# Kernel tuning notes

Measured on AMD Instinct MI355X. Metric: run time of the kernel, lower is better.

Reference implementation:

```python
import jax, jax.numpy as jnp
import numpy as np

EPS = 1e-5
NUM_HEADS = 8


def setup_inputs() -> dict:
    key = jax.random.key(0)
    ks = jax.random.split(key, 4)
    B, C, H, W = 16, 512, 32, 32
    x = jax.random.normal(ks[0], (B, C, H, W), dtype=jnp.float32)
    gn_w = jnp.ones((C,), dtype=jnp.float32)
    gn_b = jnp.zeros((C,), dtype=jnp.float32)
    # 1x1 conv weights stored as [out_ch, in_ch] (kernel dims squeezed)
    qkv_w = jax.random.normal(ks[1], (3 * C, C), dtype=jnp.float32) * (1.0 / np.sqrt(C))
    qkv_b = jnp.zeros((3 * C,), dtype=jnp.float32)
    proj_w = jax.random.normal(ks[2], (C, C), dtype=jnp.float32) * (1.0 / np.sqrt(C))
    proj_b = jnp.zeros((C,), dtype=jnp.float32)
    return {"x": x, "gn_w": gn_w, "gn_b": gn_b, "qkv_w": qkv_w,
            "qkv_b": qkv_b, "proj_w": proj_w, "proj_b": proj_b}


def _group_norm(x, w, b, groups):
    B, C, H, W = x.shape
    xg = x.reshape(B, groups, C // groups, H, W)
    mu = jnp.mean(xg, axis=(2, 3, 4), keepdims=True)
    var = jnp.var(xg, axis=(2, 3, 4), keepdims=True)
    xn = ((xg - mu) * jax.lax.rsqrt(var + EPS)).reshape(B, C, H, W)
    return xn * w[None, :, None, None] + b[None, :, None, None]


def reference(x, gn_w, gn_b, qkv_w, qkv_b, proj_w, proj_b):
    B, C, H, W = x.shape
    heads = NUM_HEADS
    d = C // heads
    residual = x
    xn = _group_norm(x, gn_w, gn_b, heads)
    # 1x1 conv == channel matmul
    qkv = jnp.einsum('oc,bchw->bohw', qkv_w, xn) + qkv_b[None, :, None, None]
    q, k, v = jnp.split(qkv, 3, axis=1)  # each [B, C, H, W]
    q = q.reshape(B, heads, d, H * W)
    k = k.reshape(B, heads, d, H * W)
    v = v.reshape(B, heads, d, H * W)
    scale = 1.0 / np.sqrt(d).astype(np.float32)
    attn = jnp.einsum('bhcn,bhcm->bhnm', q, k) * scale  # [B,h,N,N]
    attn = jax.nn.softmax(attn, axis=-1)
    out = jnp.einsum('bhnm,bhcm->bhcn', attn, v).reshape(B, C, H, W)
    out = jnp.einsum('oc,bchw->bohw', proj_w, out) + proj_b[None, :, None, None]
    return residual + out
```

## Files before the change

kernel.cpp:

```cpp
#include <hip/hip_runtime.h>
#include <hip/hip_bf16.h>
#include <math.h>

typedef short bf16x8 __attribute__((ext_vector_type(8)));
typedef short bf16x4 __attribute__((ext_vector_type(4)));
typedef float f32x4  __attribute__((ext_vector_type(4)));
#define MFMA16(a,b,c) __builtin_amdgcn_mfma_f32_16x16x32_bf16(a,b,c,0,0,0)

#if __has_builtin(__builtin_amdgcn_mfma_f32_16x16x16bf16_1k)
#define HAVE_MFMA16X16 1
#define MFMAK16(a,b,c) __builtin_amdgcn_mfma_f32_16x16x16bf16_1k(a,b,c,0,0,0)
#else
#define HAVE_MFMA16X16 0
#endif

#define EPSF 1e-5f
#define QSC 0.18033688f

#if __has_builtin(__builtin_amdgcn_exp2f)
#define EXP2(x) __builtin_amdgcn_exp2f(x)
#else
#define EXP2(x) exp2f(x)
#endif

__device__ __forceinline__ unsigned int pk2n(float a, float b){
  __hip_bfloat162 h = __float22bfloat162_rn(make_float2(a, b));
  return *reinterpret_cast<unsigned int*>(&h);
}
__device__ __forceinline__ unsigned short bfn(float f){
  __hip_bfloat16 h = __float2bfloat16(f);
  return *reinterpret_cast<unsigned short*>(&h);
}
__device__ __forceinline__ float4 ld4(const float* p){ return *reinterpret_cast<const float4*>(p); }
__device__ __forceinline__ void st4(float* p, float4 v){ *reinterpret_cast<float4*>(p) = v; }

__device__ __forceinline__ void gl_lds16(const unsigned short* g, unsigned short* l){
  __builtin_amdgcn_global_load_lds(
      (const __attribute__((address_space(1))) unsigned int*)g,
      (__attribute__((address_space(3))) unsigned int*)l, 16, 0, 0);
}

__global__ __launch_bounds__(256) void wcvt_k(const float* __restrict__ src,
                                              unsigned int* __restrict__ dst){
  int i = blockIdx.x * 256 + threadIdx.x;
  float4 v = reinterpret_cast<const float4*>(src)[i];
  uint2 r; r.x = pk2n(v.x, v.y); r.y = pk2n(v.z, v.w);
  reinterpret_cast<uint2*>(dst)[i] = r;
}

__global__ __launch_bounds__(512) void gn_fused_k(const float* __restrict__ x,
                                                  const float* __restrict__ gnw,
                                                  const float* __restrict__ gnb,
                                                  unsigned short* __restrict__ xnT){
  __shared__ float Xl[2][64*65];
  __shared__ float red[16];
  int blk = blockIdx.x;
  int b = blk >> 3, g = blk & 7;
  int tid = threadIdx.x;
  const float4* p4 = reinterpret_cast<const float4*>(x + (size_t)blk * 65536);
  float s1 = 0.f, s2 = 0.f;
  for(int i = tid; i < 16384; i += 512){
    float4 v = p4[i];
    s1 += (v.x + v.y) + (v.z + v.w);
    s2 += v.x*v.x + v.y*v.y + v.z*v.z + v.w*v.w;
  }
  #pragma unroll
  for(int off = 32; off; off >>= 1){ s1 += __shfl_xor(s1, off); s2 += __shfl_xor(s2, off); }
  if((tid & 63) == 0){ red[tid >> 6] = s1; red[8 + (tid >> 6)] = s2; }
  __syncthreads();
  float a = 0.f, b2 = 0.f;
  #pragma unroll
  for(int w = 0; w < 8; w++){ a += red[w]; b2 += red[8 + w]; }
  float mean = a * (1.f / 65536.f);
  float rstd = rsqrtf(b2 * (1.f / 65536.f) - mean * mean + EPSF);
  int half = tid >> 8, t256 = tid & 255;
  int nq = t256 & 15, rr = t256 >> 4;
  int c0 = g * 64;
  for(int it = 0; it < 8; it++){
    int n0 = (it*2 + half) * 64;
    __syncthreads();
    #pragma unroll
    for(int p = 0; p < 4; p++){
      int cl = p * 16 + rr, c = c0 + cl;
      float s = rstd * gnw[c], t = gnb[c] - mean * s;
      float4 v = ld4(x + ((size_t)(b*512 + c))*1024 + n0 + 4*nq);
      Xl[half][(4*nq+0)*65 + cl] = v.x*s + t;
      Xl[half][(4*nq+1)*65 + cl] = v.y*s + t;
      Xl[half][(4*nq+2)*65 + cl] = v.z*s + t;
      Xl[half][(4*nq+3)*65 + cl] = v.w*s + t;
    }
    __syncthreads();
    int n = t256 >> 2, cq = t256 & 3;
    float f[16];
    #pragma unroll
    for(int k = 0; k < 16; k++) f[k] = Xl[half][n*65 + 16*cq + k];
    uint4 w0, w1;
    w0.x = pk2n(f[0],f[1]);  w0.y = pk2n(f[2],f[3]);  w0.z = pk2n(f[4],f[5]);  w0.w = pk2n(f[6],f[7]);
    w1.x = pk2n(f[8],f[9]);  w1.y = pk2n(f[10],f[11]);w1.z = pk2n(f[12],f[13]);w1.w = pk2n(f[14],f[15]);
    unsigned short* dp = xnT + ((size_t)(b*1024 + n0 + n))*512 + c0 + 16*cq;
    *reinterpret_cast<uint4*>(dp)     = w0;
    *reinterpret_cast<uint4*>(dp + 8) = w1;
  }
}


__global__ __launch_bounds__(256) void qkv_mm(const unsigned short* __restrict__ A,
                                              const unsigned short* __restrict__ Bx,
                                              const float* __restrict__ bias,
                                              unsigned short* __restrict__ T,
                                              unsigned short* __restrict__ V){
  __shared__ __align__(16) unsigned short As[128*64], Bs[128*64];
  int tid = threadIdx.x;
  int n0 = blockIdx.x*128, o0 = blockIdx.y*128, b = blockIdx.z;
  int wid = tid >> 6, wr = wid >> 1, wc = wid & 1, ln = tid & 15, g = (tid >> 4) & 3;
  int l = tid & 63;
  int rsw = (ln & 7) << 3;
  int srow = 32*wid + (l >> 3);
  int scol = (((l & 7) ^ (l >> 3)) << 3);
  const unsigned short* Ag = A  + (size_t)(o0 + srow)*512 + scol;
  const unsigned short* Bg = Bx + ((size_t)(b*1024 + n0 + srow))*512 + scol;
  unsigned short* Asw = As + (32*wid)*64;
  unsigned short* Bsw = Bs + (32*wid)*64;
  f32x4 acc[4][4] = {};
  for(int k0 = 0; k0 < 512; k0 += 64){
    __syncthreads();
    #pragma unroll
    for(int c = 0; c < 4; c++){
      gl_lds16(Ag + (size_t)(8*c)*512 + k0, Asw + (8*c)*64);
      gl_lds16(Bg + (size_t)(8*c)*512 + k0, Bsw + (8*c)*64);
    }
    __syncthreads();
    #pragma unroll
    for(int kh = 0; kh < 2; kh++){
      int ro = (kh*32 + 8*g) ^ rsw;
      bf16x8 af[4], bfv[4];
      #pragma unroll
      for(int mf = 0; mf < 4; mf++)
        af[mf] = *reinterpret_cast<const bf16x8*>(&As[(wr*64 + 16*mf + ln)*64 + ro]);
      #pragma unroll
      for(int nf = 0; nf < 4; nf++)
        bfv[nf] = *reinterpret_cast<const bf16x8*>(&Bs[(wc*64 + 16*nf + ln)*64 + ro]);
      #pragma unroll
      for(int mf = 0; mf < 4; mf++)
        #pragma unroll
        for(int nf = 0; nf < 4; nf++)
          acc[mf][nf] = MFMA16(af[mf], bfv[nf], acc[mf][nf]);
    }
  }
  int obase = o0 + wr*64, nbase = n0 + wc*64;
  __syncthreads();
  unsigned short* scr = (wid < 2 ? As : Bs) + (wid & 1) * 2560;
  float sc = (obase < 512) ? QSC : 1.0f;
  if(obase < 1024){
    #pragma unroll
    for(int h2 = 0; h2 < 2; h2++){
      asm volatile("s_waitcnt lgkmcnt(0)" ::: "memory");
      __builtin_amdgcn_sched_barrier(0);
      #pragma unroll
      for(int mf2 = 0; mf2 < 2; mf2++){
        int mf = 2*h2 + mf2;
        int og = obase + 16*mf + 4*g;
        float b0 = bias[og], b1 = bias[og+1], b2 = bias[og+2], b3 = bias[og+3];
        #pragma unroll
        for(int nf = 0; nf < 4; nf++){
          uint2 pr;
          pr.x = pk2n((acc[mf][nf][0]+b0)*sc, (acc[mf][nf][1]+b1)*sc);
          pr.y = pk2n((acc[mf][nf][2]+b2)*sc, (acc[mf][nf][3]+b3)*sc);
          *reinterpret_cast<uint2*>(&scr[(16*nf + ln)*40 + 16*mf2 + 4*g]) = pr;
        }
      }
      asm volatile("s_waitcnt lgkmcnt(0)" ::: "memory");
      __builtin_amdgcn_sched_barrier(0);
      const unsigned short* rp = &scr[l*40];
      uint4 r0 = *reinterpret_cast<const uint4*>(rp);
      uint4 r1 = *reinterpret_cast<const uint4*>(rp+8);
      uint4 r2 = *reinterpret_cast<const uint4*>(rp+16);
      uint4 r3 = *reinterpret_cast<const uint4*>(rp+24);
      unsigned short* dp = T + ((size_t)(b*1024 + nbase + l))*1024 + obase + 32*h2;
      *reinterpret_cast<uint4*>(dp)    = r0;
      *reinterpret_cast<uint4*>(dp+8)  = r1;
      *reinterpret_cast<uint4*>(dp+16) = r2;
      *reinterpret_cast<uint4*>(dp+24) = r3;
    }
  } else {
    #pragma unroll
    for(int h2 = 0; h2 < 2; h2++){
      asm volatile("s_waitcnt lgkmcnt(0)" ::: "memory");
      __builtin_amdgcn_sched_barrier(0);
      #pragma unroll
      for(int nf2 = 0; nf2 < 2; nf2++){
        int nf = 2*h2 + nf2;
        #pragma unroll
        for(int mf = 0; mf < 4; mf++){
          int og = obase + 16*mf + 4*g;
          #pragma unroll
          for(int r = 0; r < 4; r++)
            scr[(16*mf + 4*g + r)*40 + 16*nf2 + ln] = bfn(acc[mf][nf][r] + bias[og+r]);
        }
      }
      asm volatile("s_waitcnt lgkmcnt(0)" ::: "memory");
      __builtin_amdgcn_sched_barrier(0);
      const unsigned short* rp = &scr[l*40];
      uint4 r0 = *reinterpret_cast<const uint4*>(rp);
      uint4 r1 = *reinterpret_cast<const uint4*>(rp+8);
      uint4 r2 = *reinterpret_cast<const uint4*>(rp+16);
      uint4 r3 = *reinterpret_cast<const uint4*>(rp+24);
      unsigned short* dp = V + ((size_t)(b*512 + obase - 1024 + l))*1024 + nbase + 32*h2;
      *reinterpret_cast<uint4*>(dp)    = r0;
      *reinterpret_cast<uint4*>(dp+8)  = r1;
      *reinterpret_cast<uint4*>(dp+16) = r2;
      *reinterpret_cast<uint4*>(dp+24) = r3;
    }
  }
}

__global__ __launch_bounds__(256) void attn_bf_k(const unsigned short* __restrict__ T,
                                                 const unsigned short* __restrict__ V,
                                                 unsigned short* __restrict__ attT){
  __shared__ __align__(16) unsigned short KT[2][64*64];
  __shared__ __align__(16) unsigned short Vt[2][64*64];
#if !HAVE_MFMA16X16
  __shared__ __align__(16) unsigned int   Pl[4*16*32];
#endif
  int tid = threadIdx.x;
  int id = blockIdx.x;
  int bh = (id >> 7) * 8 + (id & 7);
  int n0 = ((id >> 3) & 15) * 64;
  int b = bh >> 3, h = bh & 7;
  int wq = tid >> 6, ln = tid & 15, g = (tid >> 4) & 3;
  int l = tid & 63;
  int nl = n0 + wq*16 + ln;
  const unsigned short* Tb = T + ((size_t)b << 20);
  bf16x8 qf0 = *reinterpret_cast<const bf16x8*>(Tb + (size_t)nl*1024 + h*64 + 8*g);
  bf16x8 qf1 = *reinterpret_cast<const bf16x8*>(Tb + (size_t)nl*1024 + h*64 + 32 + 8*g);
  f32x4 acc[4] = {};
  float l_part = 0.f;
  const unsigned short* kg = Tb + 512 + h*64;
  const unsigned short* vg = V + ((size_t)(b*512 + h*64))*1024;
  int swz  = (((l & 7) << 3) ^ ((l >> 3) << 3));
  const unsigned short* ksrc = kg + (size_t)(wq*16 + (l>>3))*1024 + swz;
  const unsigned short* vsrc = vg + (size_t)(wq*16 + (l>>3))*1024 + swz;
  int rsw = (ln & 7) << 3;
  int ro0 = (8*g) ^ rsw, ro1 = (32 + 8*g) ^ rsw;
#if HAVE_MFMA16X16
  int vcol[4];
  #pragma unroll
  for(int mf = 0; mf < 4; mf++)
    vcol[mf] = (((2*mf + (g>>1)) ^ (ln & 7)) << 3) + 4*(g & 1);
#else
  int pbase = wq*512 + ln*32;
  int psw = (ln & 7) << 2;
#endif
  {
    unsigned short* kb = &KT[0][wq*16*64];
    unsigned short* vb = &Vt[0][wq*16*64];
    gl_lds16(ksrc,            kb);
    gl_lds16(ksrc + 8*1024,   kb + 8*64);
    gl_lds16(vsrc,            vb);
    gl_lds16(vsrc + 8*1024,   vb + 8*64);
  }
  __syncthreads();
  for(int t = 0; t < 16; t++){
    int buf = t & 1;
    if(t < 15){
      int m1 = (t + 1) * 64;
      unsigned short* kb = &KT[buf^1][wq*16*64];
      unsigned short* vb = &Vt[buf^1][wq*16*64];
      gl_lds16(ksrc + (size_t)m1*1024,          kb);
      gl_lds16(ksrc + (size_t)(m1+8)*1024,      kb + 8*64);
      gl_lds16(vsrc + m1,                       vb);
      gl_lds16(vsrc + 8*1024 + m1,              vb + 8*64);
    }
    f32x4 sf[4];
    #pragma unroll
    for(int mf = 0; mf < 4; mf++){
      bf16x8 a0 = *reinterpret_cast<const bf16x8*>(&KT[buf][(16*mf + ln)*64 + ro0]);
      bf16x8 a1 = *reinterpret_cast<const bf16x8*>(&KT[buf][(16*mf + ln)*64 + ro1]);
      f32x4 z = {0.f, 0.f, 0.f, 0.f};
      z = MFMA16(a0, qf0, z);
      sf[mf] = MFMA16(a1, qf1, z);
    }
    float p[16];
    #pragma unroll
    for(int mf = 0; mf < 4; mf++)
      #pragma unroll
      for(int r = 0; r < 4; r++){
        float v = EXP2(sf[mf][r]);
        p[mf*4 + r] = v;
        l_part += v;
      }
#if HAVE_MFMA16X16
    bf16x4 pb[4];
    #pragma unroll
    for(int mf = 0; mf < 4; mf++){
      union { uint2 u; bf16x4 h; } cv;
      cv.u.x = pk2n(p[4*mf + 0], p[4*mf + 1]);
      cv.u.y = pk2n(p[4*mf + 2], p[4*mf + 3]);
      pb[mf] = cv.h;
    }
    #pragma unroll
    for(int cf = 0; cf < 4; cf++){
      #pragma unroll
      for(int mf = 0; mf < 4; mf++){
        bf16x4 va = *reinterpret_cast<const bf16x4*>(&Vt[buf][(16*cf + ln)*64 + vcol[mf]]);
        acc[cf] = MFMAK16(va, pb[mf], acc[cf]);
      }
    }
#else
    #pragma unroll
    for(int mt = 0; mt < 4; mt++){
      Pl[pbase + ((8*mt + 2*g + 0) ^ psw)] = pk2n(p[4*mt + 0], p[4*mt + 1]);
      Pl[pbase + ((8*mt + 2*g + 1) ^ psw)] = pk2n(p[4*mt + 2], p[4*mt + 3]);
    }
    asm volatile("s_waitcnt lgkmcnt(0)" ::: "memory");
    __builtin_amdgcn_sched_barrier(0);
    union { uint4 u; bf16x8 hv; } pb0, pb1;
    pb0.u = *reinterpret_cast<const uint4*>(&Pl[pbase + ((4*g) ^ psw)]);
    pb1.u = *reinterpret_cast<const uint4*>(&Pl[pbase + ((16 + 4*g) ^ psw)]);
    #pragma unroll
    for(int cf = 0; cf < 4; cf++){
      bf16x8 v0 = *reinterpret_cast<const bf16x8*>(&Vt[buf][(16*cf + ln)*64 + ro0]);
      bf16x8 v1 = *reinterpret_cast<const bf16x8*>(&Vt[buf][(16*cf + ln)*64 + ro1]);
      acc[cf] = MFMA16(v0, pb0.hv, acc[cf]);
      acc[cf] = MFMA16(v1, pb1.hv, acc[cf]);
    }
#endif
    __syncthreads();
  }
  float lsum = l_part;
  lsum += __shfl_xor(lsum, 16);
  lsum += __shfl_xor(lsum, 32);
  float inv = 1.f / lsum;
  unsigned short* op = attT + ((size_t)(b*1024 + nl))*512 + h*64;
  #pragma unroll
  for(int cf = 0; cf < 4; cf++){
    uint2 pr;
    pr.x = pk2n(acc[cf][0]*inv, acc[cf][1]*inv);
    pr.y = pk2n(acc[cf][2]*inv, acc[cf][3]*inv);
    *reinterpret_cast<uint2*>(op + 16*cf + 4*g) = pr;
  }
}

__global__ __launch_bounds__(256) void proj_mm(const unsigned short* __restrict__ A,
                                               const unsigned short* __restrict__ Bx,
                                               const float* __restrict__ bias,
                                               const float* __restrict__ resid,
                                               float* __restrict__ out){
  __shared__ __align__(16) unsigned short As[128*64], Bs[128*64];
  int tid = threadIdx.x;
  int n0 = blockIdx.x*128, o0 = blockIdx.y*128, b = blockIdx.z;
  int wid = tid >> 6, wr = wid >> 1, wc = wid & 1, ln = tid & 15, g = (tid >> 4) & 3;
  int l = tid & 63;
  int rsw = (ln & 7) << 3;
  int srow = 32*wid + (l >> 3);
  int scol = (((l & 7) ^ (l >> 3)) << 3);
  const unsigned short* Ag = A  + (size_t)(o0 + srow)*512 + scol;
  const unsigned short* Bg = Bx + ((size_t)(b*1024 + n0 + srow))*512 + scol;
  unsigned short* Asw = As + (32*wid)*64;
  unsigned short* Bsw = Bs + (32*wid)*64;
  f32x4 acc[4][4] = {};
  for(int k0 = 0; k0 < 512; k0 += 64){
    __syncthreads();
    #pragma unroll
    for(int c = 0; c < 4; c++){
      gl_lds16(Ag + (size_t)(8*c)*512 + k0, Asw + (8*c)*64);
      gl_lds16(Bg + (size_t)(8*c)*512 + k0, Bsw + (8*c)*64);
    }
    __syncthreads();
    #pragma unroll
    for(int kh = 0; kh < 2; kh++){
      int ro = (kh*32 + 8*g) ^ rsw;
      bf16x8 af[4], bfv[4];
      #pragma unroll
      for(int mf = 0; mf < 4; mf++)
        af[mf] = *reinterpret_cast<const bf16x8*>(&As[(wr*64 + 16*mf + ln)*64 + ro]);
      #pragma unroll
      for(int nf = 0; nf < 4; nf++)
        bfv[nf] = *reinterpret_cast<const bf16x8*>(&Bs[(wc*64 + 16*nf + ln)*64 + ro]);
      #pragma unroll
      for(int mf = 0; mf < 4; mf++)
        #pragma unroll
        for(int nf = 0; nf < 4; nf++)
          acc[mf][nf] = MFMA16(af[mf], bfv[nf], acc[mf][nf]);
    }
  }
  #pragma unroll
  for(int mf = 0; mf < 4; mf++)
    #pragma unroll
    for(int r = 0; r < 4; r++){
      int o = o0 + wr*64 + 16*mf + 4*g + r;
      float bo = bias[o];
      #pragma unroll
      for(int nf = 0; nf < 4; nf++){
        int n = n0 + wc*64 + 16*nf + ln;
        size_t off = ((size_t)(b*512 + o))*1024 + n;
        out[off] = acc[mf][nf][r] + bo + resid[off];
      }
    }
}

extern "C" void kernel_launch(void* const* d_in, const int* in_sizes, int n_in,
                              void* d_out, int out_size, void* d_ws, size_t ws_size,
                              hipStream_t stream){
  const float* x     = (const float*)d_in[0];
  const float* gnw   = (const float*)d_in[1];
  const float* gnb   = (const float*)d_in[2];
  const float* qkvw  = (const float*)d_in[3];
  const float* qkvb  = (const float*)d_in[4];
  const float* projw = (const float*)d_in[5];
  const float* projb = (const float*)d_in[6];
  float* out = (float*)d_out;

  char* w = (char*)d_ws;
  unsigned short* wqb = (unsigned short*)w;  w += (size_t)1536*512*2;
  unsigned short* wpb = (unsigned short*)w;  w += (size_t)512*512*2;
  unsigned short* xnT = (unsigned short*)w;  w += (size_t)16*1024*512*2;
  unsigned short* Tqk = (unsigned short*)w;  w += (size_t)16*1024*1024*2;
  unsigned short* Vb  = (unsigned short*)w;  w += (size_t)16*512*1024*2;
  unsigned short* attT = (unsigned short*)w; w += (size_t)16*1024*512*2;

  hipLaunchKernelGGL(wcvt_k, dim3(768), dim3(256), 0, stream, qkvw, (unsigned int*)wqb);
  hipLaunchKernelGGL(wcvt_k, dim3(256), dim3(256), 0, stream, projw, (unsigned int*)wpb);
  hipLaunchKernelGGL(gn_fused_k, dim3(128), dim3(512), 0, stream, x, gnw, gnb, xnT);
  hipLaunchKernelGGL(qkv_mm, dim3(8, 12, 16), dim3(256), 0, stream, wqb, xnT, qkvb, Tqk, Vb);
  hipLaunchKernelGGL(attn_bf_k, dim3(2048), dim3(256), 0, stream, Tqk, Vb, attT);
  hipLaunchKernelGGL(proj_mm, dim3(8, 4, 16), dim3(256), 0, stream, wpb, attT, projb, x, out);
}
```

Baseline: 160.1 us.

## Double-buffer GEMM K tiles and drop the K16 MFMA attention path

The QKV and projection GEMMs now use two 32-wide K buffers in shared memory. The next tile's async load is issued before computing the current one, with one barrier per step instead of two, to hide global load latency. The attention kernel drops the 16x16x16 MFMA variant and always stages P through LDS so it can use 16x16x32 MFMAs. This adds more loop iterations and an LDS round trip for P in exchange for fewer, larger matrix instructions.

```diff
diff --git a/kernel.cpp b/kernel.cpp
--- a/kernel.cpp
+++ b/kernel.cpp
@@ -3,16 +3,8 @@
 #include <math.h>
 
 typedef short bf16x8 __attribute__((ext_vector_type(8)));
-typedef short bf16x4 __attribute__((ext_vector_type(4)));
 typedef float f32x4  __attribute__((ext_vector_type(4)));
 #define MFMA16(a,b,c) __builtin_amdgcn_mfma_f32_16x16x32_bf16(a,b,c,0,0,0)
-
-#if __has_builtin(__builtin_amdgcn_mfma_f32_16x16x16bf16_1k)
-#define HAVE_MFMA16X16 1
-#define MFMAK16(a,b,c) __builtin_amdgcn_mfma_f32_16x16x16bf16_1k(a,b,c,0,0,0)
-#else
-#define HAVE_MFMA16X16 0
-#endif
 
 #define EPSF 1e-5f
 #define QSC 0.18033688f
@@ -109,47 +101,49 @@
                                               const float* __restrict__ bias,
                                               unsigned short* __restrict__ T,
                                               unsigned short* __restrict__ V){
-  __shared__ __align__(16) unsigned short As[128*64], Bs[128*64];
+  __shared__ __align__(16) unsigned short As[2][128*32], Bs[2][128*32];
   int tid = threadIdx.x;
   int n0 = blockIdx.x*128, o0 = blockIdx.y*128, b = blockIdx.z;
   int wid = tid >> 6, wr = wid >> 1, wc = wid & 1, ln = tid & 15, g = (tid >> 4) & 3;
   int l = tid & 63;
-  int rsw = (ln & 7) << 3;
-  int srow = 32*wid + (l >> 3);
-  int scol = (((l & 7) ^ (l >> 3)) << 3);
+  int srow = 32*wid + (l >> 2);
+  int scol = 8*((l & 3) ^ ((l >> 3) & 3));
   const unsigned short* Ag = A  + (size_t)(o0 + srow)*512 + scol;
   const unsigned short* Bg = Bx + ((size_t)(b*1024 + n0 + srow))*512 + scol;
-  unsigned short* Asw = As + (32*wid)*64;
-  unsigned short* Bsw = Bs + (32*wid)*64;
+  int ro = 8*(g ^ ((ln >> 1) & 3));
   f32x4 acc[4][4] = {};
-  for(int k0 = 0; k0 < 512; k0 += 64){
-    __syncthreads();
-    #pragma unroll
-    for(int c = 0; c < 4; c++){
-      gl_lds16(Ag + (size_t)(8*c)*512 + k0, Asw + (8*c)*64);
-      gl_lds16(Bg + (size_t)(8*c)*512 + k0, Bsw + (8*c)*64);
-    }
-    __syncthreads();
-    #pragma unroll
-    for(int kh = 0; kh < 2; kh++){
-      int ro = (kh*32 + 8*g) ^ rsw;
-      bf16x8 af[4], bfv[4];
-      #pragma unroll
-      for(int mf = 0; mf < 4; mf++)
-        af[mf] = *reinterpret_cast<const bf16x8*>(&As[(wr*64 + 16*mf + ln)*64 + ro]);
+  #pragma unroll
+  for(int c = 0; c < 2; c++){
+    gl_lds16(Ag + (size_t)(16*c)*512, &As[0][(32*wid + 16*c)*32]);
+    gl_lds16(Bg + (size_t)(16*c)*512, &Bs[0][(32*wid + 16*c)*32]);
+  }
+  __syncthreads();
+  for(int t = 0; t < 16; t++){
+    int buf = t & 1;
+    if(t < 15){
+      int k1 = (t + 1) * 32;
+      #pragma unroll
+      for(int c = 0; c < 2; c++){
+        gl_lds16(Ag + (size_t)(16*c)*512 + k1, &As[buf^1][(32*wid + 16*c)*32]);
+        gl_lds16(Bg + (size_t)(16*c)*512 + k1, &Bs[buf^1][(32*wid + 16*c)*32]);
+      }
+    }
+    bf16x8 af[4], bfv[4];
+    #pragma unroll
+    for(int mf = 0; mf < 4; mf++)
+      af[mf] = *reinterpret_cast<const bf16x8*>(&As[buf][(wr*64 + 16*mf + ln)*32 + ro]);
+    #pragma unroll
+    for(int nf = 0; nf < 4; nf++)
+      bfv[nf] = *reinterpret_cast<const bf16x8*>(&Bs[buf][(wc*64 + 16*nf + ln)*32 + ro]);
+    #pragma unroll
+    for(int mf = 0; mf < 4; mf++)
       #pragma unroll
       for(int nf = 0; nf < 4; nf++)
-        bfv[nf] = *reinterpret_cast<const bf16x8*>(&Bs[(wc*64 + 16*nf + ln)*64 + ro]);
-      #pragma unroll
-      for(int mf = 0; mf < 4; mf++)
-        #pragma unroll
-        for(int nf = 0; nf < 4; nf++)
-          acc[mf][nf] = MFMA16(af[mf], bfv[nf], acc[mf][nf]);
-    }
+        acc[mf][nf] = MFMA16(af[mf], bfv[nf], acc[mf][nf]);
+    __syncthreads();
   }
   int obase = o0 + wr*64, nbase = n0 + wc*64;
-  __syncthreads();
-  unsigned short* scr = (wid < 2 ? As : Bs) + (wid & 1) * 2560;
+  unsigned short* scr = (wid < 2 ? &As[0][0] : &Bs[0][0]) + (wid & 1) * 2560;
   float sc = (obase < 512) ? QSC : 1.0f;
   if(obase < 1024){
     #pragma unroll
@@ -219,9 +213,7 @@
                                                  unsigned short* __restrict__ attT){
   __shared__ __align__(16) unsigned short KT[2][64*64];
   __shared__ __align__(16) unsigned short Vt[2][64*64];
-#if !HAVE_MFMA16X16
   __shared__ __align__(16) unsigned int   Pl[4*16*32];
-#endif
   int tid = threadIdx.x;
   int id = blockIdx.x;
   int bh = (id >> 7) * 8 + (id & 7);
@@ -237,20 +229,13 @@
   float l_part = 0.f;
   const unsigned short* kg = Tb + 512 + h*64;
   const unsigned short* vg = V + ((size_t)(b*512 + h*64))*1024;
+  int pbase = wq*512 + ln*32;
+  int psw = (ln & 7) << 2;
   int swz  = (((l & 7) << 3) ^ ((l >> 3) << 3));
   const unsigned short* ksrc = kg + (size_t)(wq*16 + (l>>3))*1024 + swz;
   const unsigned short* vsrc = vg + (size_t)(wq*16 + (l>>3))*1024 + swz;
   int rsw = (ln & 7) << 3;
   int ro0 = (8*g) ^ rsw, ro1 = (32 + 8*g) ^ rsw;
-#if HAVE_MFMA16X16
-  int vcol[4];
-  #pragma unroll
-  for(int mf = 0; mf < 4; mf++)
-    vcol[mf] = (((2*mf + (g>>1)) ^ (ln & 7)) << 3) + 4*(g & 1);
-#else
-  int pbase = wq*512 + ln*32;
-  int psw = (ln & 7) << 2;
-#endif
   {
     unsigned short* kb = &KT[0][wq*16*64];
     unsigned short* vb = &Vt[0][wq*16*64];
@@ -289,24 +274,6 @@
         p[mf*4 + r] = v;
         l_part += v;
       }
-#if HAVE_MFMA16X16
-    bf16x4 pb[4];
-    #pragma unroll
-    for(int mf = 0; mf < 4; mf++){
-      union { uint2 u; bf16x4 h; } cv;
-      cv.u.x = pk2n(p[4*mf + 0], p[4*mf + 1]);
-      cv.u.y = pk2n(p[4*mf + 2], p[4*mf + 3]);
-      pb[mf] = cv.h;
-    }
-    #pragma unroll
-    for(int cf = 0; cf < 4; cf++){
-      #pragma unroll
-      for(int mf = 0; mf < 4; mf++){
-        bf16x4 va = *reinterpret_cast<const bf16x4*>(&Vt[buf][(16*cf + ln)*64 + vcol[mf]]);
-        acc[cf] = MFMAK16(va, pb[mf], acc[cf]);
-      }
-    }
-#else
     #pragma unroll
     for(int mt = 0; mt < 4; mt++){
       Pl[pbase + ((8*mt + 2*g + 0) ^ psw)] = pk2n(p[4*mt + 0], p[4*mt + 1]);
@@ -324,7 +291,6 @@
       acc[cf] = MFMA16(v0, pb0.hv, acc[cf]);
       acc[cf] = MFMA16(v1, pb1.hv, acc[cf]);
     }
-#endif
     __syncthreads();
   }
   float lsum = l_part;
@@ -346,43 +312,46 @@
                                                const float* __restrict__ bias,
                                                const float* __restrict__ resid,
                                                float* __restrict__ out){
-  __shared__ __align__(16) unsigned short As[128*64], Bs[128*64];
+  __shared__ __align__(16) unsigned short As[2][128*32], Bs[2][128*32];
   int tid = threadIdx.x;
   int n0 = blockIdx.x*128, o0 = blockIdx.y*128, b = blockIdx.z;
   int wid = tid >> 6, wr = wid >> 1, wc = wid & 1, ln = tid & 15, g = (tid >> 4) & 3;
   int l = tid & 63;
-  int rsw = (ln & 7) << 3;
-  int srow = 32*wid + (l >> 3);
-  int scol = (((l & 7) ^ (l >> 3)) << 3);
+  int srow = 32*wid + (l >> 2);
+  int scol = 8*((l & 3) ^ ((l >> 3) & 3));
   const unsigned short* Ag = A  + (size_t)(o0 + srow)*512 + scol;
   const unsigned short* Bg = Bx + ((size_t)(b*1024 + n0 + srow))*512 + scol;
-  unsigned short* Asw = As + (32*wid)*64;
-  unsigned short* Bsw = Bs + (32*wid)*64;
+  int ro = 8*(g ^ ((ln >> 1) & 3));
   f32x4 acc[4][4] = {};
-  for(int k0 = 0; k0 < 512; k0 += 64){
-    __syncthreads();
-    #pragma unroll
-    for(int c = 0; c < 4; c++){
-      gl_lds16(Ag + (size_t)(8*c)*512 + k0, Asw + (8*c)*64);
-      gl_lds16(Bg + (size_t)(8*c)*512 + k0, Bsw + (8*c)*64);
-    }
-    __syncthreads();
-    #pragma unroll
-    for(int kh = 0; kh < 2; kh++){
-      int ro = (kh*32 + 8*g) ^ rsw;
-      bf16x8 af[4], bfv[4];
-      #pragma unroll
-      for(int mf = 0; mf < 4; mf++)
-        af[mf] = *reinterpret_cast<const bf16x8*>(&As[(wr*64 + 16*mf + ln)*64 + ro]);
+  #pragma unroll
+  for(int c = 0; c < 2; c++){
+    gl_lds16(Ag + (size_t)(16*c)*512, &As[0][(32*wid + 16*c)*32]);
+    gl_lds16(Bg + (size_t)(16*c)*512, &Bs[0][(32*wid + 16*c)*32]);
+  }
+  __syncthreads();
+  for(int t = 0; t < 16; t++){
+    int buf = t & 1;
+    if(t < 15){
+      int k1 = (t + 1) * 32;
+      #pragma unroll
+      for(int c = 0; c < 2; c++){
+        gl_lds16(Ag + (size_t)(16*c)*512 + k1, &As[buf^1][(32*wid + 16*c)*32]);
+        gl_lds16(Bg + (size_t)(16*c)*512 + k1, &Bs[buf^1][(32*wid + 16*c)*32]);
+      }
+    }
+    bf16x8 af[4], bfv[4];
+    #pragma unroll
+    for(int mf = 0; mf < 4; mf++)
+      af[mf] = *reinterpret_cast<const bf16x8*>(&As[buf][(wr*64 + 16*mf + ln)*32 + ro]);
+    #pragma unroll
+    for(int nf = 0; nf < 4; nf++)
+      bfv[nf] = *reinterpret_cast<const bf16x8*>(&Bs[buf][(wc*64 + 16*nf + ln)*32 + ro]);
+    #pragma unroll
+    for(int mf = 0; mf < 4; mf++)
       #pragma unroll
       for(int nf = 0; nf < 4; nf++)
-        bfv[nf] = *reinterpret_cast<const bf16x8*>(&Bs[(wc*64 + 16*nf + ln)*64 + ro]);
-      #pragma unroll
-      for(int mf = 0; mf < 4; mf++)
-        #pragma unroll
-        for(int nf = 0; nf < 4; nf++)
-          acc[mf][nf] = MFMA16(af[mf], bfv[nf], acc[mf][nf]);
-    }
+        acc[mf][nf] = MFMA16(af[mf], bfv[nf], acc[mf][nf]);
+    __syncthreads();
   }
   #pragma unroll
   for(int mf = 0; mf < 4; mf++)
```

After: 163.2 us. About the same (+1.9%).

## Process two query tiles per attention block to reuse staged K/V tiles

Applied to the files above, without the earlier changes.

Each attention block now handles 128 query rows, as two 64-row sub-tiles that share every K/V tile loaded into LDS. That halves the global-to-LDS traffic and the barrier count per query row, and the grid shrinks from 2048 to 1024 blocks. The 16x16x16 MFMA path that kept P in registers is dropped in favour of always routing P through LDS with the 16x16x32 MFMA. Launch bounds now request 4 blocks per CU. The cost is more registers, fewer blocks, and an extra LDS round trip for P on targets that used to take the register path.

```diff
diff --git a/kernel.cpp b/kernel.cpp
--- a/kernel.cpp
+++ b/kernel.cpp
@@ -3,16 +3,8 @@
 #include <math.h>
 
 typedef short bf16x8 __attribute__((ext_vector_type(8)));
-typedef short bf16x4 __attribute__((ext_vector_type(4)));
 typedef float f32x4  __attribute__((ext_vector_type(4)));
 #define MFMA16(a,b,c) __builtin_amdgcn_mfma_f32_16x16x32_bf16(a,b,c,0,0,0)
-
-#if __has_builtin(__builtin_amdgcn_mfma_f32_16x16x16bf16_1k)
-#define HAVE_MFMA16X16 1
-#define MFMAK16(a,b,c) __builtin_amdgcn_mfma_f32_16x16x16bf16_1k(a,b,c,0,0,0)
-#else
-#define HAVE_MFMA16X16 0
-#endif
 
 #define EPSF 1e-5f
 #define QSC 0.18033688f
@@ -214,43 +206,34 @@
   }
 }
 
-__global__ __launch_bounds__(256) void attn_bf_k(const unsigned short* __restrict__ T,
-                                                 const unsigned short* __restrict__ V,
-                                                 unsigned short* __restrict__ attT){
+__global__ __launch_bounds__(256, 4) void attn_bf_k(const unsigned short* __restrict__ T,
+                                                    const unsigned short* __restrict__ V,
+                                                    unsigned short* __restrict__ attT){
   __shared__ __align__(16) unsigned short KT[2][64*64];
   __shared__ __align__(16) unsigned short Vt[2][64*64];
-#if !HAVE_MFMA16X16
   __shared__ __align__(16) unsigned int   Pl[4*16*32];
-#endif
   int tid = threadIdx.x;
   int id = blockIdx.x;
-  int bh = (id >> 7) * 8 + (id & 7);
-  int n0 = ((id >> 3) & 15) * 64;
-  int b = bh >> 3, h = bh & 7;
+  int h = id & 7, n0 = ((id >> 3) & 7) * 128, b = id >> 6;
   int wq = tid >> 6, ln = tid & 15, g = (tid >> 4) & 3;
   int l = tid & 63;
-  int nl = n0 + wq*16 + ln;
+  int nl0 = n0 + wq*16 + ln, nl1 = nl0 + 64;
   const unsigned short* Tb = T + ((size_t)b << 20);
-  bf16x8 qf0 = *reinterpret_cast<const bf16x8*>(Tb + (size_t)nl*1024 + h*64 + 8*g);
-  bf16x8 qf1 = *reinterpret_cast<const bf16x8*>(Tb + (size_t)nl*1024 + h*64 + 32 + 8*g);
-  f32x4 acc[4] = {};
-  float l_part = 0.f;
+  bf16x8 qa0 = *reinterpret_cast<const bf16x8*>(Tb + (size_t)nl0*1024 + h*64 + 8*g);
+  bf16x8 qa1 = *reinterpret_cast<const bf16x8*>(Tb + (size_t)nl0*1024 + h*64 + 32 + 8*g);
+  bf16x8 qb0 = *reinterpret_cast<const bf16x8*>(Tb + (size_t)nl1*1024 + h*64 + 8*g);
+  bf16x8 qb1 = *reinterpret_cast<const bf16x8*>(Tb + (size_t)nl1*1024 + h*64 + 32 + 8*g);
+  f32x4 acc[2][4] = {};
+  float l_part[2] = {0.f, 0.f};
   const unsigned short* kg = Tb + 512 + h*64;
   const unsigned short* vg = V + ((size_t)(b*512 + h*64))*1024;
+  int pbase = wq*512 + ln*32;
+  int psw = (ln & 7) << 2;
   int swz  = (((l & 7) << 3) ^ ((l >> 3) << 3));
   const unsigned short* ksrc = kg + (size_t)(wq*16 + (l>>3))*1024 + swz;
   const unsigned short* vsrc = vg + (size_t)(wq*16 + (l>>3))*1024 + swz;
   int rsw = (ln & 7) << 3;
   int ro0 = (8*g) ^ rsw, ro1 = (32 + 8*g) ^ rsw;
-#if HAVE_MFMA16X16
-  int vcol[4];
-  #pragma unroll
-  for(int mf = 0; mf < 4; mf++)
-    vcol[mf] = (((2*mf + (g>>1)) ^ (ln & 7)) << 3) + 4*(g & 1);
-#else
-  int pbase = wq*512 + ln*32;
-  int psw = (ln & 7) << 2;
-#endif
   {
     unsigned short* kb = &KT[0][wq*16*64];
     unsigned short* vb = &Vt[0][wq*16*64];
@@ -271,73 +254,66 @@
       gl_lds16(vsrc + m1,                       vb);
       gl_lds16(vsrc + 8*1024 + m1,              vb + 8*64);
     }
-    f32x4 sf[4];
-    #pragma unroll
-    for(int mf = 0; mf < 4; mf++){
-      bf16x8 a0 = *reinterpret_cast<const bf16x8*>(&KT[buf][(16*mf + ln)*64 + ro0]);
-      bf16x8 a1 = *reinterpret_cast<const bf16x8*>(&KT[buf][(16*mf + ln)*64 + ro1]);
-      f32x4 z = {0.f, 0.f, 0.f, 0.f};
-      z = MFMA16(a0, qf0, z);
-      sf[mf] = MFMA16(a1, qf1, z);
-    }
-    float p[16];
-    #pragma unroll
-    for(int mf = 0; mf < 4; mf++)
-      #pragma unroll
-      for(int r = 0; r < 4; r++){
-        float v = EXP2(sf[mf][r]);
-        p[mf*4 + r] = v;
-        l_part += v;
-      }
-#if HAVE_MFMA16X16
-    bf16x4 pb[4];
-    #pragma unroll
-    for(int mf = 0; mf < 4; mf++){
-      union { uint2 u; bf16x4 h; } cv;
-      cv.u.x = pk2n(p[4*mf + 0], p[4*mf + 1]);
-      cv.u.y = pk2n(p[4*mf + 2], p[4*mf + 3]);
-      pb[mf] = cv.h;
-    }
+    #pragma unroll
+    for(int sub = 0; sub < 2; sub++){
+      bf16x8 q0 = sub ? qb0 : qa0;
+      bf16x8 q1 = sub ? qb1 : qa1;
+      f32x4 sf[4];
+      #pragma unroll
+      for(int mf = 0; mf < 4; mf++){
+        bf16x8 a0 = *reinterpret_cast<const bf16x8*>(&KT[buf][(16*mf + ln)*64 + ro0]);
+        bf16x8 a1 = *reinterpret_cast<const bf16x8*>(&KT[buf][(16*mf + ln)*64 + ro1]);
+        f32x4 z = {0.f, 0.f, 0.f, 0.f};
+        z = MFMA16(a0, q0, z);
+        sf[mf] = MFMA16(a1, q1, z);
+      }
+      float p[16];
+      float lp = 0.f;
+      #pragma unroll
+      for(int mf = 0; mf < 4; mf++)
+        #pragma unroll
+        for(int r = 0; r < 4; r++){
+          float v = EXP2(sf[mf][r]);
+          p[mf*4 + r] = v;
+          lp += v;
+        }
+      l_part[sub] += lp;
+      #pragma unroll
+      for(int mt = 0; mt < 4; mt++){
+        Pl[pbase + ((8*mt + 2*g + 0) ^ psw)] = pk2n(p[4*mt + 0], p[4*mt + 1]);
+        Pl[pbase + ((8*mt + 2*g + 1) ^ psw)] = pk2n(p[4*mt + 2], p[4*mt + 3]);
+      }
+      asm volatile("s_waitcnt lgkmcnt(0)" ::: "memory");
+      __builtin_amdgcn_sched_barrier(0);
+      union { uint4 u; bf16x8 hv; } pb0, pb1;
+      pb0.u = *reinterpret_cast<const uint4*>(&Pl[pbase + ((4*g) ^ psw)]);
+      pb1.u = *reinterpret_cast<const uint4*>(&Pl[pbase + ((16 + 4*g) ^ psw)]);
+      #pragma unroll
+      for(int cf = 0; cf < 4; cf++){
+        bf16x8 v0 = *reinterpret_cast<const bf16x8*>(&Vt[buf][(16*cf + ln)*64 + ro0]);
+        bf16x8 v1 = *reinterpret_cast<const bf16x8*>(&Vt[buf][(16*cf + ln)*64 + ro1]);
+        acc[sub][cf] = MFMA16(v0, pb0.hv, acc[sub][cf]);
+        acc[sub][cf] = MFMA16(v1, pb1.hv, acc[sub][cf]);
+      }
+      __builtin_amdgcn_sched_barrier(0);
+    }
+    __syncthreads();
+  }
+  #pragma unroll
+  for(int sub = 0; sub < 2; sub++){
+    float lsum = l_part[sub];
+    lsum += __shfl_xor(lsum, 16);
+    lsum += __shfl_xor(lsum, 32);
+    float inv = 1.f / lsum;
+    int nl = sub ? nl1 : nl0;
+    unsigned short* op = attT + ((size_t)(b*1024 + nl))*512 + h*64;
     #pragma unroll
     for(int cf = 0; cf < 4; cf++){
-      #pragma unroll
-      for(int mf = 0; mf < 4; mf++){
-        bf16x4 va = *reinterpret_cast<const bf16x4*>(&Vt[buf][(16*cf + ln)*64 + vcol[mf]]);
-        acc[cf] = MFMAK16(va, pb[mf], acc[cf]);
-      }
-    }
-#else
-    #pragma unroll
-    for(int mt = 0; mt < 4; mt++){
-      Pl[pbase + ((8*mt + 2*g + 0) ^ psw)] = pk2n(p[4*mt + 0], p[4*mt + 1]);
-      Pl[pbase + ((8*mt + 2*g + 1) ^ psw)] = pk2n(p[4*mt + 2], p[4*mt + 3]);
-    }
-    asm volatile("s_waitcnt lgkmcnt(0)" ::: "memory");
-    __builtin_amdgcn_sched_barrier(0);
-    union { uint4 u; bf16x8 hv; } pb0, pb1;
-    pb0.u = *reinterpret_cast<const uint4*>(&Pl[pbase + ((4*g) ^ psw)]);
-    pb1.u = *reinterpret_cast<const uint4*>(&Pl[pbase + ((16 + 4*g) ^ psw)]);
-    #pragma unroll
-    for(int cf = 0; cf < 4; cf++){
-      bf16x8 v0 = *reinterpret_cast<const bf16x8*>(&Vt[buf][(16*cf + ln)*64 + ro0]);
-      bf16x8 v1 = *reinterpret_cast<const bf16x8*>(&Vt[buf][(16*cf + ln)*64 + ro1]);
-      acc[cf] = MFMA16(v0, pb0.hv, acc[cf]);
-      acc[cf] = MFMA16(v1, pb1.hv, acc[cf]);
-    }
-#endif
-    __syncthreads();
-  }
-  float lsum = l_part;
-  lsum += __shfl_xor(lsum, 16);
-  lsum += __shfl_xor(lsum, 32);
-  float inv = 1.f / lsum;
-  unsigned short* op = attT + ((size_t)(b*1024 + nl))*512 + h*64;
-  #pragma unroll
-  for(int cf = 0; cf < 4; cf++){
-    uint2 pr;
-    pr.x = pk2n(acc[cf][0]*inv, acc[cf][1]*inv);
-    pr.y = pk2n(acc[cf][2]*inv, acc[cf][3]*inv);
-    *reinterpret_cast<uint2*>(op + 16*cf + 4*g) = pr;
+      uint2 pr;
+      pr.x = pk2n(acc[sub][cf][0]*inv, acc[sub][cf][1]*inv);
+      pr.y = pk2n(acc[sub][cf][2]*inv, acc[sub][cf][3]*inv);
+      *reinterpret_cast<uint2*>(op + 16*cf + 4*g) = pr;
+    }
   }
 }
 
@@ -423,6 +399,6 @@
   hipLaunchKernelGGL(wcvt_k, dim3(256), dim3(256), 0, stream, projw, (unsigned int*)wpb);
   hipLaunchKernelGGL(gn_fused_k, dim3(128), dim3(512), 0, stream, x, gnw, gnb, xnT);
   hipLaunchKernelGGL(qkv_mm, dim3(8, 12, 16), dim3(256), 0, stream, wqb, xnT, qkvb, Tqk, Vb);
-  hipLaunchKernelGGL(attn_bf_k, dim3(2048), dim3(256), 0, stream, Tqk, Vb, attT);
+  hipLaunchKernelGGL(attn_bf_k, dim3(1024), dim3(256), 0, stream, Tqk, Vb, attT);
   hipLaunchKernelGGL(proj_mm, dim3(8, 4, 16), dim3(256), 0, stream, wpb, attT, projb, x, out);
 }
```

New measurement: 168.0 us. +5.0%, slower.

## Drop 16x16x16 MFMA path, compute softmax row sums via MFMA with ones, add setprio

Applied to the files above, without the earlier changes.

Removes the 16x16x16 bf16 MFMA path so P always goes through LDS as bf16x8 fragments for the 16x16x32 MFMA. The softmax denominator is now accumulated by an extra MFMA against a vector of ones instead of scalar adds and cross-lane shuffles. s_setprio is raised around the MFMA blocks to favour matrix issue across waves. The cost is an LDS round trip for P on every tile and an extra MFMA pair per tile. The row sum now comes from the bf16-rounded P values that also feed the P·V product.

```diff
diff --git a/kernel.cpp b/kernel.cpp
--- a/kernel.cpp
+++ b/kernel.cpp
@@ -3,16 +3,8 @@
 #include <math.h>
 
 typedef short bf16x8 __attribute__((ext_vector_type(8)));
-typedef short bf16x4 __attribute__((ext_vector_type(4)));
 typedef float f32x4  __attribute__((ext_vector_type(4)));
 #define MFMA16(a,b,c) __builtin_amdgcn_mfma_f32_16x16x32_bf16(a,b,c,0,0,0)
-
-#if __has_builtin(__builtin_amdgcn_mfma_f32_16x16x16bf16_1k)
-#define HAVE_MFMA16X16 1
-#define MFMAK16(a,b,c) __builtin_amdgcn_mfma_f32_16x16x16bf16_1k(a,b,c,0,0,0)
-#else
-#define HAVE_MFMA16X16 0
-#endif
 
 #define EPSF 1e-5f
 #define QSC 0.18033688f
@@ -219,9 +211,7 @@
                                                  unsigned short* __restrict__ attT){
   __shared__ __align__(16) unsigned short KT[2][64*64];
   __shared__ __align__(16) unsigned short Vt[2][64*64];
-#if !HAVE_MFMA16X16
   __shared__ __align__(16) unsigned int   Pl[4*16*32];
-#endif
   int tid = threadIdx.x;
   int id = blockIdx.x;
   int bh = (id >> 7) * 8 + (id & 7);
@@ -234,23 +224,18 @@
   bf16x8 qf0 = *reinterpret_cast<const bf16x8*>(Tb + (size_t)nl*1024 + h*64 + 8*g);
   bf16x8 qf1 = *reinterpret_cast<const bf16x8*>(Tb + (size_t)nl*1024 + h*64 + 32 + 8*g);
   f32x4 acc[4] = {};
-  float l_part = 0.f;
+  f32x4 accl = {};
+  const short one_bf = (short)0x3F80;
+  bf16x8 ones8 = {one_bf,one_bf,one_bf,one_bf,one_bf,one_bf,one_bf,one_bf};
   const unsigned short* kg = Tb + 512 + h*64;
   const unsigned short* vg = V + ((size_t)(b*512 + h*64))*1024;
+  int pbase = wq*512 + ln*32;
+  int psw = (ln & 7) << 2;
   int swz  = (((l & 7) << 3) ^ ((l >> 3) << 3));
   const unsigned short* ksrc = kg + (size_t)(wq*16 + (l>>3))*1024 + swz;
   const unsigned short* vsrc = vg + (size_t)(wq*16 + (l>>3))*1024 + swz;
   int rsw = (ln & 7) << 3;
   int ro0 = (8*g) ^ rsw, ro1 = (32 + 8*g) ^ rsw;
-#if HAVE_MFMA16X16
-  int vcol[4];
-  #pragma unroll
-  for(int mf = 0; mf < 4; mf++)
-    vcol[mf] = (((2*mf + (g>>1)) ^ (ln & 7)) << 3) + 4*(g & 1);
-#else
-  int pbase = wq*512 + ln*32;
-  int psw = (ln & 7) << 2;
-#endif
   {
     unsigned short* kb = &KT[0][wq*16*64];
     unsigned short* vb = &Vt[0][wq*16*64];
@@ -272,6 +257,7 @@
       gl_lds16(vsrc + 8*1024 + m1,              vb + 8*64);
     }
     f32x4 sf[4];
+    __builtin_amdgcn_s_setprio(1);
     #pragma unroll
     for(int mf = 0; mf < 4; mf++){
       bf16x8 a0 = *reinterpret_cast<const bf16x8*>(&KT[buf][(16*mf + ln)*64 + ro0]);
@@ -280,33 +266,13 @@
       z = MFMA16(a0, qf0, z);
       sf[mf] = MFMA16(a1, qf1, z);
     }
+    __builtin_amdgcn_s_setprio(0);
     float p[16];
     #pragma unroll
     for(int mf = 0; mf < 4; mf++)
       #pragma unroll
-      for(int r = 0; r < 4; r++){
-        float v = EXP2(sf[mf][r]);
-        p[mf*4 + r] = v;
-        l_part += v;
-      }
-#if HAVE_MFMA16X16
-    bf16x4 pb[4];
-    #pragma unroll
-    for(int mf = 0; mf < 4; mf++){
-      union { uint2 u; bf16x4 h; } cv;
-      cv.u.x = pk2n(p[4*mf + 0], p[4*mf + 1]);
-      cv.u.y = pk2n(p[4*mf + 2], p[4*mf + 3]);
-      pb[mf] = cv.h;
-    }
-    #pragma unroll
-    for(int cf = 0; cf < 4; cf++){
-      #pragma unroll
-      for(int mf = 0; mf < 4; mf++){
-        bf16x4 va = *reinterpret_cast<const bf16x4*>(&Vt[buf][(16*cf + ln)*64 + vcol[mf]]);
-        acc[cf] = MFMAK16(va, pb[mf], acc[cf]);
-      }
-    }
-#else
+      for(int r = 0; r < 4; r++)
+        p[mf*4 + r] = EXP2(sf[mf][r]);
     #pragma unroll
     for(int mt = 0; mt < 4; mt++){
       Pl[pbase + ((8*mt + 2*g + 0) ^ psw)] = pk2n(p[4*mt + 0], p[4*mt + 1]);
@@ -317,6 +283,9 @@
     union { uint4 u; bf16x8 hv; } pb0, pb1;
     pb0.u = *reinterpret_cast<const uint4*>(&Pl[pbase + ((4*g) ^ psw)]);
     pb1.u = *reinterpret_cast<const uint4*>(&Pl[pbase + ((16 + 4*g) ^ psw)]);
+    __builtin_amdgcn_s_setprio(1);
+    accl = MFMA16(ones8, pb0.hv, accl);
+    accl = MFMA16(ones8, pb1.hv, accl);
     #pragma unroll
     for(int cf = 0; cf < 4; cf++){
       bf16x8 v0 = *reinterpret_cast<const bf16x8*>(&Vt[buf][(16*cf + ln)*64 + ro0]);
@@ -324,13 +293,10 @@
       acc[cf] = MFMA16(v0, pb0.hv, acc[cf]);
       acc[cf] = MFMA16(v1, pb1.hv, acc[cf]);
     }
-#endif
-    __syncthreads();
-  }
-  float lsum = l_part;
-  lsum += __shfl_xor(lsum, 16);
-  lsum += __shfl_xor(lsum, 32);
-  float inv = 1.f / lsum;
+    __builtin_amdgcn_s_setprio(0);
+    __syncthreads();
+  }
+  float inv = 1.f / accl[0];
   unsigned short* op = attT + ((size_t)(b*1024 + nl))*512 + h*64;
   #pragma unroll
   for(int cf = 0; cf < 4; cf++){
```

Result: no change. 159.7 us (-0.2%).
